# Performance work log

Measured on AMD Instinct MI355X. Metric: run time of the kernel, lower is better.

## Reference

```python
import jax, jax.numpy as jnp
import numpy as np
import math

B, D, S, C, H = 8192, 512, 5, 2048, 4

def setup_inputs() -> dict:
    key = jax.random.key(0)
    ks = jax.random.split(key, 8)
    return {
        "features": jax.random.normal(ks[0], (B, D), dtype=jnp.float32),
        "logits": jax.random.normal(ks[1], (S, B, C), dtype=jnp.float32),
        "scale_feats": jax.random.normal(ks[2], (S, B, D), dtype=jnp.float32),
        "Wq": jax.random.normal(ks[3], (D, D), dtype=jnp.float32) * 0.02,
        "bq": jnp.zeros((D,), jnp.float32),
        "Wk": jax.random.normal(ks[4], (D, D), dtype=jnp.float32) * 0.02,
        "bk": jnp.zeros((D,), jnp.float32),
        "Wv": jax.random.normal(ks[5], (D, D), dtype=jnp.float32) * 0.02,
        "bv": jnp.zeros((D,), jnp.float32),
        "scale_emb": jax.random.normal(ks[6], (S, D), dtype=jnp.float32) * 0.02,
        "temperature": jnp.float32(0.07),
        "attn_w": jnp.ones((3,), jnp.float32) / 3.0,
    }

def reference(features, logits, scale_feats, Wq, bq, Wk, bk, Wv, bv, scale_emb, temperature, attn_w):
    b, d = features.shape
    s = scale_feats.shape[0]
    hd = d // H
    t = jnp.abs(temperature)

    # ---- multihead attention over scales (V is computed in torch but unused) ----
    Q = (features @ Wq + bq).reshape(b, H, hd)                      # [B,H,hd]
    sf_emb = scale_feats + scale_emb[:, None, :]                    # [S,B,D]
    K = (sf_emb @ Wk + bk).reshape(s, b, H, hd)                     # [S,B,H,hd]
    scores = jnp.einsum('bhd,sbhd->bhs', Q, K) / jnp.float32(math.sqrt(hd))
    attn_mha = jax.nn.softmax(scores / t, axis=-1).mean(axis=1)     # [B,S]

    # ---- geometric (angular) attention ----
    fn = features / jnp.linalg.norm(features, axis=-1, keepdims=True).clip(1e-12)
    sfn = scale_feats / jnp.linalg.norm(scale_feats, axis=-1, keepdims=True).clip(1e-12)
    cos_sim = jnp.einsum('bd,sbd->bs', fn, sfn)                     # [B,S]
    angles = jnp.arccos(jnp.clip(cos_sim, -1.0 + 1e-7, 1.0 - 1e-7))
    attn_geo = jax.nn.softmax(jnp.exp(-angles / t), axis=-1)        # [B,S]

    # ---- Cayley-Menger volume-proxy attention ----
    # simplex points: [features, scale_feat, cos(a)*f + sin(a)*s for a in {pi/4, pi/2, 3pi/4}]
    c = jnp.float32(math.sqrt(0.5))
    cf = jnp.array([1.0, 0.0, c, 0.0, -c], jnp.float32)             # coeffs on features
    cs = jnp.array([0.0, 1.0, c, 1.0, c], jnp.float32)              # coeffs on scale_feat
    simplex = (cf[None, :, None, None] * features[None, None] +
               cs[None, :, None, None] * scale_feats[:, None])      # [S,5,B,D]
    norms = jnp.sum(simplex * simplex, axis=-1)                     # [S,5,B]
    gram = jnp.einsum('spbd,sqbd->spqb', simplex, simplex)          # [S,5,5,B]
    distsq = norms[:, :, None] + norms[:, None, :] - 2.0 * gram     # [S,5,5,B]
    volumes = distsq.mean(axis=(1, 2)).T                            # [B,S]
    attn_cay = jax.nn.softmax(volumes / t, axis=-1)

    # ---- fuse attention types ----
    w = jax.nn.softmax(attn_w, axis=0)
    combined = w[0] * attn_mha + w[1] * attn_geo + w[2] * attn_cay  # [B,S]
    combined = combined / combined.sum(axis=-1, keepdims=True)

    combined_logits = jnp.einsum('bs,sbc->bc', combined, logits)    # [B,C]
    return (combined_logits, combined)
```

## Files before the change

### kernel.cpp

```cpp
#include <hip/hip_runtime.h>
#include <math.h>

#define B_N 8192
#define D_N 512
#define S_N 5
#define C_N 2048
#define H_N 4

typedef __attribute__((ext_vector_type(8))) short bf16x8;
typedef __attribute__((ext_vector_type(4))) float floatx4;

__device__ __forceinline__ float bf2f(short u) {
  union { unsigned int i; float f; } c;
  c.i = ((unsigned int)(unsigned short)u) << 16;
  return c.f;
}
__device__ __forceinline__ short f2bf(float f) {
  union { float f; unsigned int i; } c; c.f = f;
  unsigned int x = c.i;
  x += 0x7fffu + ((x >> 16) & 1u);
  return (short)(x >> 16);
}

__global__ __launch_bounds__(256) void k_cvt_f(const float* __restrict__ f,
                                               short* __restrict__ fbf, int n8) {
  int i = blockIdx.x * 256 + threadIdx.x;
  if (i >= n8) return;
  const floatx4* p = (const floatx4*)(f + (size_t)i * 8);
  floatx4 a = p[0], b = p[1];
  bf16x8 o;
  o[0] = f2bf(a[0]); o[1] = f2bf(a[1]); o[2] = f2bf(a[2]); o[3] = f2bf(a[3]);
  o[4] = f2bf(b[0]); o[5] = f2bf(b[1]); o[6] = f2bf(b[2]); o[7] = f2bf(b[3]);
  *(bf16x8*)(fbf + (size_t)i * 8) = o;
}

__global__ __launch_bounds__(256) void k_cvt_w(const float* __restrict__ Wq,
                                               const float* __restrict__ Wk,
                                               short* __restrict__ WqT,
                                               short* __restrict__ Wkb) {
  int o = blockIdx.x * 256 + threadIdx.x;
  if (blockIdx.x < 1024) {
    int n = o >> 9, k = o & 511;
    WqT[(size_t)n * 512 + k] = f2bf(Wq[(size_t)k * 512 + n]);
  } else {
    int o2 = o - 262144;
    Wkb[o2] = f2bf(Wk[o2]);
  }
}

__device__ __forceinline__ void gll(const short* g, short* l) {
  __builtin_amdgcn_global_load_lds(
      (const __attribute__((address_space(1))) unsigned int*)(g),
      (__attribute__((address_space(3))) unsigned int*)(l), 16, 0, 0);
}

__global__ __launch_bounds__(256) void k_gemm(
    const short* __restrict__ A, int lda,
    const short* __restrict__ BT, int ldb,
    short* __restrict__ O, int ldo,
    const float* __restrict__ bias, int K, int z_koff, int z_coff) {
  __shared__ __align__(16) short As[2][4096];
  __shared__ __align__(16) short Bs[2][4096];

  const int tid = threadIdx.x;
  const int lane = tid & 63;
  const int wid = tid >> 6;
  const int wr = wid >> 1, wc = wid & 1;
  const int row0 = blockIdx.y * 128;
  const int col0 = blockIdx.x * 128;
  const int z = blockIdx.z;
  const int koff = z * z_koff;
  const int ocoff = z * z_coff;

  const int r1 = tid >> 2, hk = tid & 3;
  const short* Ag1 = A + (size_t)(row0 + r1) * lda + koff + hk * 8;
  const short* Ag2 = A + (size_t)(row0 + 64 + r1) * lda + koff + hk * 8;
  const short* Bg1 = BT + (size_t)(col0 + r1) * ldb + koff + hk * 8;
  const short* Bg2 = BT + (size_t)(col0 + 64 + r1) * ldb + koff + hk * 8;

  floatx4 acc[4][4];
  const floatx4 zero = {0.0f, 0.0f, 0.0f, 0.0f};
#pragma unroll
  for (int m = 0; m < 4; ++m)
#pragma unroll
    for (int n = 0; n < 4; ++n) acc[m][n] = zero;

  const int NT = K >> 5;
  int cur = 0;

  auto stage = [&](int q, int kb) {
    gll(Ag1 + kb, &As[q][tid * 8]);
    gll(Ag2 + kb, &As[q][tid * 8 + 2048]);
    gll(Bg1 + kb, &Bs[q][tid * 8]);
    gll(Bg2 + kb, &Bs[q][tid * 8 + 2048]);
  };

  stage(0, 0);
  __syncthreads();

  for (int t = 0; t < NT; ++t) {
    if (t + 1 < NT) stage(cur ^ 1, (t + 1) * 32);
    bf16x8 af[4], bfr[4];
#pragma unroll
    for (int m = 0; m < 4; ++m)
      af[m] = *(const bf16x8*)&As[cur][(wr * 64 + m * 16 + (lane & 15)) * 32 + (lane >> 4) * 8];
#pragma unroll
    for (int n = 0; n < 4; ++n)
      bfr[n] = *(const bf16x8*)&Bs[cur][(wc * 64 + n * 16 + (lane & 15)) * 32 + (lane >> 4) * 8];
#pragma unroll
    for (int m = 0; m < 4; ++m)
#pragma unroll
      for (int n = 0; n < 4; ++n)
        acc[m][n] = __builtin_amdgcn_mfma_f32_16x16x32_bf16(af[m], bfr[n], acc[m][n], 0, 0, 0);
    __syncthreads();
    cur ^= 1;
  }

#pragma unroll
  for (int m = 0; m < 4; ++m) {
    int rowb = row0 + wr * 64 + m * 16 + (lane >> 4) * 4;
#pragma unroll
    for (int n = 0; n < 4; ++n) {
      int lcol = col0 + wc * 64 + n * 16 + (lane & 15);
      float bv = bias ? bias[lcol] : 0.0f;
      int ocol = ocoff + lcol;
#pragma unroll
      for (int j = 0; j < 4; ++j) {
        O[(size_t)(rowb + j) * ldo + ocol] = f2bf(acc[m][n][j] + bv);
      }
    }
  }
}

__global__ __launch_bounds__(256) void k_stats(
    const float* __restrict__ f, const float* __restrict__ sf,
    const float* __restrict__ emb, const short* __restrict__ Qbf,
    const short* __restrict__ Rbf, const float* __restrict__ bk,
    const float* __restrict__ temp, const float* __restrict__ attn_w,
    float* __restrict__ comb_out) {
  const int lane = threadIdx.x & 63;
  const int wid = threadIdx.x >> 6;
  const int b = blockIdx.x * 4 + wid;
  const int a0 = lane * 8;

  const floatx4* fp = (const floatx4*)(f + (size_t)b * D_N + a0);
  floatx4 fA = fp[0], fB = fp[1];
  float fv[8];
#pragma unroll
  for (int j = 0; j < 4; ++j) { fv[j] = fA[j]; fv[4 + j] = fB[j]; }
  float ffp = 0;
#pragma unroll
  for (int j = 0; j < 8; ++j) ffp += fv[j] * fv[j];

  bf16x8 qv = *(const bf16x8*)(Qbf + (size_t)b * D_N + a0);
  float qbkp = 0;
#pragma unroll
  for (int j = 0; j < 8; ++j) qbkp += bf2f(qv[j]) * bk[a0 + j];

  float rf[H_N][8];
#pragma unroll
  for (int h = 0; h < H_N; ++h) {
    bf16x8 rv = *(const bf16x8*)(Rbf + (size_t)b * 2048 + h * 512 + a0);
#pragma unroll
    for (int j = 0; j < 8; ++j) rf[h][j] = bf2f(rv[j]);
  }

  const int myh = lane >> 4;
  float fs_[S_N], ss_[S_N], sc_[S_N][H_N];

#pragma unroll
  for (int s = 0; s < S_N; ++s) {
    const floatx4* sp = (const floatx4*)(sf + ((size_t)s * B_N + b) * D_N + a0);
    floatx4 sA = sp[0], sB = sp[1];
    const floatx4* ep = (const floatx4*)(emb + (size_t)s * D_N + a0);
    floatx4 eA = ep[0], eB = ep[1];
    float sv[8], se[8];
#pragma unroll
    for (int j = 0; j < 4; ++j) {
      sv[j] = sA[j]; sv[4 + j] = sB[j];
      se[j] = sA[j] + eA[j]; se[4 + j] = sB[j] + eB[j];
    }
    float fsp = 0, ssp = 0;
    float scp[H_N];
#pragma unroll
    for (int h = 0; h < H_N; ++h) scp[h] = (myh == h) ? qbkp : 0.0f;
#pragma unroll
    for (int j = 0; j < 8; ++j) {
      fsp += fv[j] * sv[j];
      ssp += sv[j] * sv[j];
#pragma unroll
      for (int h = 0; h < H_N; ++h) scp[h] += se[j] * rf[h][j];
    }
#pragma unroll
    for (int o = 1; o < 64; o <<= 1) {
      fsp += __shfl_xor(fsp, o, 64);
      ssp += __shfl_xor(ssp, o, 64);
#pragma unroll
      for (int h = 0; h < H_N; ++h) scp[h] += __shfl_xor(scp[h], o, 64);
    }
    fs_[s] = fsp; ss_[s] = ssp;
#pragma unroll
    for (int h = 0; h < H_N; ++h) sc_[s][h] = scp[h];
  }
  float ffv = ffp;
#pragma unroll
  for (int o = 1; o < 64; o <<= 1) ffv += __shfl_xor(ffv, o, 64);

  const float t = fabsf(temp[0]);

  float amha[S_N] = {0, 0, 0, 0, 0};
  const float inv_mha = 1.0f / (sqrtf(128.0f) * t);
#pragma unroll
  for (int h = 0; h < H_N; ++h) {
    float lg[S_N];
#pragma unroll
    for (int s = 0; s < S_N; ++s) lg[s] = sc_[s][h] * inv_mha;
    float mx = lg[0];
#pragma unroll
    for (int s = 1; s < S_N; ++s) mx = fmaxf(mx, lg[s]);
    float e[S_N], sum = 0;
#pragma unroll
    for (int s = 0; s < S_N; ++s) { e[s] = __expf(lg[s] - mx); sum += e[s]; }
    float isum = 0.25f / sum;
#pragma unroll
    for (int s = 0; s < S_N; ++s) amha[s] += e[s] * isum;
  }

  float ageo[S_N];
  {
    const float nf = fmaxf(sqrtf(ffv), 1e-12f);
    float g[S_N];
#pragma unroll
    for (int s = 0; s < S_N; ++s) {
      float ns = fmaxf(sqrtf(ss_[s]), 1e-12f);
      float cs0 = fs_[s] / (nf * ns);
      cs0 = fminf(fmaxf(cs0, -1.0f + 1e-7f), 1.0f - 1e-7f);
      g[s] = __expf(-acosf(cs0) / t);
    }
    float mx = g[0];
#pragma unroll
    for (int s = 1; s < S_N; ++s) mx = fmaxf(mx, g[s]);
    float sum = 0;
#pragma unroll
    for (int s = 0; s < S_N; ++s) { ageo[s] = __expf(g[s] - mx); sum += ageo[s]; }
#pragma unroll
    for (int s = 0; s < S_N; ++s) ageo[s] /= sum;
  }

  float acay[S_N];
  {
    const float SQ2 = 1.41421356237309515f;
    const float Aff = 0.72f;
    const float Ass = 0.72f - 0.32f * SQ2;
    const float Afs = -(8.0f + 4.0f * SQ2) / 25.0f;
    float lg[S_N];
#pragma unroll
    for (int s = 0; s < S_N; ++s)
      lg[s] = (Aff * ffv + Ass * ss_[s] + Afs * fs_[s]) / t;
    float mx = lg[0];
#pragma unroll
    for (int s = 1; s < S_N; ++s) mx = fmaxf(mx, lg[s]);
    float sum = 0;
#pragma unroll
    for (int s = 0; s < S_N; ++s) { acay[s] = __expf(lg[s] - mx); sum += acay[s]; }
#pragma unroll
    for (int s = 0; s < S_N; ++s) acay[s] /= sum;
  }

  float w0 = attn_w[0], w1 = attn_w[1], w2 = attn_w[2];
  float wm = fmaxf(w0, fmaxf(w1, w2));
  float e0 = __expf(w0 - wm), e1 = __expf(w1 - wm), e2 = __expf(w2 - wm);
  float wsum = e0 + e1 + e2;
  w0 = e0 / wsum; w1 = e1 / wsum; w2 = e2 / wsum;

  float cb[S_N], csum = 0;
#pragma unroll
  for (int s = 0; s < S_N; ++s) {
    cb[s] = w0 * amha[s] + w1 * ageo[s] + w2 * acay[s];
    csum += cb[s];
  }
  float ic = 1.0f / csum;
  if (lane == 0) {
#pragma unroll
    for (int s = 0; s < S_N; ++s) comb_out[(size_t)b * S_N + s] = cb[s] * ic;
  }
}

__global__ __launch_bounds__(256) void k_mix(const float* __restrict__ logits,
                                             const float* __restrict__ comb,
                                             float* __restrict__ out) {
  const int b = blockIdx.x;
  const int c0 = threadIdx.x * 8;
  float cs[S_N];
#pragma unroll
  for (int s = 0; s < S_N; ++s) cs[s] = comb[(size_t)b * S_N + s];
  floatx4 accA = {0, 0, 0, 0}, accB = {0, 0, 0, 0};
#pragma unroll
  for (int s = 0; s < S_N; ++s) {
    const float* lp = logits + ((size_t)s * B_N + b) * C_N + c0;
    floatx4 lA = *(const floatx4*)lp;
    floatx4 lB = *(const floatx4*)(lp + 4);
    accA += lA * cs[s];
    accB += lB * cs[s];
  }
  float* op = out + (size_t)b * C_N + c0;
  *(floatx4*)op = accA;
  *(floatx4*)(op + 4) = accB;
}

extern "C" void kernel_launch(void* const* d_in, const int* in_sizes, int n_in,
                              void* d_out, int out_size, void* d_ws, size_t ws_size,
                              hipStream_t stream) {
  const float* features = (const float*)d_in[0];
  const float* logits   = (const float*)d_in[1];
  const float* sf       = (const float*)d_in[2];
  const float* Wq       = (const float*)d_in[3];
  const float* bq       = (const float*)d_in[4];
  const float* Wk       = (const float*)d_in[5];
  const float* bk       = (const float*)d_in[6];
  const float* emb      = (const float*)d_in[9];
  const float* temp     = (const float*)d_in[10];
  const float* attn_w   = (const float*)d_in[11];

  float* out  = (float*)d_out;
  float* comb = out + (size_t)B_N * C_N;

  char* w = (char*)d_ws;
  short* fbf = (short*)(w);
  short* Qbf = (short*)(w + 8388608);
  short* Rbf = (short*)(w + 16777216);
  short* WqT = (short*)(w + 50331648);
  short* Wkb = (short*)(w + 50855936);

  k_cvt_f<<<dim3(2048), dim3(256), 0, stream>>>(features, fbf, 524288);
  k_cvt_w<<<dim3(2048), dim3(256), 0, stream>>>(Wq, Wk, WqT, Wkb);
  k_gemm<<<dim3(4, 64, 1), dim3(256), 0, stream>>>(fbf, 512, WqT, 512, Qbf, 512,
                                                   bq, 512, 0, 0);
  k_gemm<<<dim3(4, 64, 4), dim3(256), 0, stream>>>(Qbf, 512, Wkb, 512, Rbf, 2048,
                                                   (const float*)nullptr, 128, 128, 512);
  k_stats<<<dim3(2048), dim3(256), 0, stream>>>(features, sf, emb, Qbf, Rbf, bk,
                                                temp, attn_w, comb);
  k_mix<<<dim3(8192), dim3(256), 0, stream>>>(logits, comb, out);
}
```

Before: 158.4 us.

## Fuse feature conversion, both GEMMs and stats into one per-row-block kernel

Replaces the feature conversion, the Q GEMM, the Q·Wk^T GEMM and the stats kernel with a single kernel. Each block handles 32 rows, keeps the bf16 features and Q in swizzled LDS, and computes per-head K·Q scores on the fly against bf16 scale-feature tiles. This removes the global round-trips of fbf, Qbf and the large Rbf intermediate plus several launches. The cost is only 256 blocks with heavy LDS use and weight fragments read straight from global/L2 without LDS staging, so occupancy and GEMM efficiency may drop.

Measured after the change: 157.2 us. No clear change (-0.8%).

```diff
diff --git a/kernel.cpp b/kernel.cpp
--- a/kernel.cpp
+++ b/kernel.cpp
@@ -6,6 +6,7 @@
 #define S_N 5
 #define C_N 2048
 #define H_N 4
+#define RB 32
 
 typedef __attribute__((ext_vector_type(8))) short bf16x8;
 typedef __attribute__((ext_vector_type(4))) float floatx4;
@@ -21,23 +22,17 @@
   x += 0x7fffu + ((x >> 16) & 1u);
   return (short)(x >> 16);
 }
-
-__global__ __launch_bounds__(256) void k_cvt_f(const float* __restrict__ f,
-                                               short* __restrict__ fbf, int n8) {
-  int i = blockIdx.x * 256 + threadIdx.x;
-  if (i >= n8) return;
-  const floatx4* p = (const floatx4*)(f + (size_t)i * 8);
-  floatx4 a = p[0], b = p[1];
-  bf16x8 o;
-  o[0] = f2bf(a[0]); o[1] = f2bf(a[1]); o[2] = f2bf(a[2]); o[3] = f2bf(a[3]);
-  o[4] = f2bf(b[0]); o[5] = f2bf(b[1]); o[6] = f2bf(b[2]); o[7] = f2bf(b[3]);
-  *(bf16x8*)(fbf + (size_t)i * 8) = o;
-}
-
-__global__ __launch_bounds__(256) void k_cvt_w(const float* __restrict__ Wq,
-                                               const float* __restrict__ Wk,
-                                               short* __restrict__ WqT,
-                                               short* __restrict__ Wkb) {
+__device__ __forceinline__ unsigned long long pack4(float a, float b, float c, float d) {
+  return (unsigned long long)(unsigned short)f2bf(a)
+       | ((unsigned long long)(unsigned short)f2bf(b) << 16)
+       | ((unsigned long long)(unsigned short)f2bf(c) << 32)
+       | ((unsigned long long)(unsigned short)f2bf(d) << 48);
+}
+
+__global__ __launch_bounds__(256) void k_prep(const float* __restrict__ Wq,
+                                              const float* __restrict__ Wk,
+                                              short* __restrict__ WqT,
+                                              short* __restrict__ Wkb) {
   int o = blockIdx.x * 256 + threadIdx.x;
   if (blockIdx.x < 1024) {
     int n = o >> 9, k = o & 511;
@@ -48,241 +43,318 @@
   }
 }
 
-__device__ __forceinline__ void gll(const short* g, short* l) {
-  __builtin_amdgcn_global_load_lds(
-      (const __attribute__((address_space(1))) unsigned int*)(g),
-      (__attribute__((address_space(3))) unsigned int*)(l), 16, 0, 0);
-}
-
-__global__ __launch_bounds__(256) void k_gemm(
-    const short* __restrict__ A, int lda,
-    const short* __restrict__ BT, int ldb,
-    short* __restrict__ O, int ldo,
-    const float* __restrict__ bias, int K, int z_koff, int z_coff) {
-  __shared__ __align__(16) short As[2][4096];
-  __shared__ __align__(16) short Bs[2][4096];
+__global__ __launch_bounds__(256, 2) void k_mega(
+    const float* __restrict__ f, const float* __restrict__ sf,
+    const float* __restrict__ emb, const short* __restrict__ WqT,
+    const short* __restrict__ Wkb, const float* __restrict__ bq,
+    const float* __restrict__ bk, const float* __restrict__ temp,
+    const float* __restrict__ attn_w, float* __restrict__ comb_out) {
+  __shared__ __align__(16) short uni[21120];
+  __shared__ __align__(16) short Qbf[16384];
+  __shared__ float ffLds[RB];
+  __shared__ float qtLds[RB][H_N];
+  __shared__ float scLds[RB][H_N][S_N];
+  __shared__ float fsLds[S_N][RB];
+  __shared__ float ssLds[S_N][RB];
 
   const int tid = threadIdx.x;
   const int lane = tid & 63;
   const int wid = tid >> 6;
-  const int wr = wid >> 1, wc = wid & 1;
-  const int row0 = blockIdx.y * 128;
-  const int col0 = blockIdx.x * 128;
-  const int z = blockIdx.z;
-  const int koff = z * z_koff;
-  const int ocoff = z * z_coff;
-
-  const int r1 = tid >> 2, hk = tid & 3;
-  const short* Ag1 = A + (size_t)(row0 + r1) * lda + koff + hk * 8;
-  const short* Ag2 = A + (size_t)(row0 + 64 + r1) * lda + koff + hk * 8;
-  const short* Bg1 = BT + (size_t)(col0 + r1) * ldb + koff + hk * 8;
-  const short* Bg2 = BT + (size_t)(col0 + 64 + r1) * ldb + koff + hk * 8;
-
-  floatx4 acc[4][4];
-  const floatx4 zero = {0.0f, 0.0f, 0.0f, 0.0f};
-#pragma unroll
-  for (int m = 0; m < 4; ++m)
-#pragma unroll
-    for (int n = 0; n < 4; ++n) acc[m][n] = zero;
-
-  const int NT = K >> 5;
-  int cur = 0;
-
-  auto stage = [&](int q, int kb) {
-    gll(Ag1 + kb, &As[q][tid * 8]);
-    gll(Ag2 + kb, &As[q][tid * 8 + 2048]);
-    gll(Bg1 + kb, &Bs[q][tid * 8]);
-    gll(Bg2 + kb, &Bs[q][tid * 8 + 2048]);
-  };
-
-  stage(0, 0);
+  const int b0 = blockIdx.x * RB;
+
+  {
+    const int r0 = tid >> 3;
+    const int c0 = (tid & 7) * 64;
+    const float* fp = f + (size_t)(b0 + r0) * D_N + c0;
+    float ffp = 0.0f;
+#pragma unroll
+    for (int i = 0; i < 8; ++i) {
+      floatx4 a = *(const floatx4*)(fp + i * 8);
+      floatx4 b = *(const floatx4*)(fp + i * 8 + 4);
+      ffp += a[0]*a[0] + a[1]*a[1] + a[2]*a[2] + a[3]*a[3];
+      ffp += b[0]*b[0] + b[1]*b[1] + b[2]*b[2] + b[3]*b[3];
+      bf16x8 o;
+      o[0]=f2bf(a[0]); o[1]=f2bf(a[1]); o[2]=f2bf(a[2]); o[3]=f2bf(a[3]);
+      o[4]=f2bf(b[0]); o[5]=f2bf(b[1]); o[6]=f2bf(b[2]); o[7]=f2bf(b[3]);
+      int byteoff = (r0 * 1024 + (c0 + i * 8) * 2) ^ ((r0 & 7) << 4);
+      *(bf16x8*)((char*)uni + byteoff) = o;
+    }
+    ffp += __shfl_xor(ffp, 1, 64);
+    ffp += __shfl_xor(ffp, 2, 64);
+    ffp += __shfl_xor(ffp, 4, 64);
+    if ((tid & 7) == 0) ffLds[r0] = ffp;
+  }
   __syncthreads();
 
-  for (int t = 0; t < NT; ++t) {
-    if (t + 1 < NT) stage(cur ^ 1, (t + 1) * 32);
-    bf16x8 af[4], bfr[4];
-#pragma unroll
-    for (int m = 0; m < 4; ++m)
-      af[m] = *(const bf16x8*)&As[cur][(wr * 64 + m * 16 + (lane & 15)) * 32 + (lane >> 4) * 8];
-#pragma unroll
-    for (int n = 0; n < 4; ++n)
-      bfr[n] = *(const bf16x8*)&Bs[cur][(wc * 64 + n * 16 + (lane & 15)) * 32 + (lane >> 4) * 8];
-#pragma unroll
-    for (int m = 0; m < 4; ++m)
-#pragma unroll
-      for (int n = 0; n < 4; ++n)
-        acc[m][n] = __builtin_amdgcn_mfma_f32_16x16x32_bf16(af[m], bfr[n], acc[m][n], 0, 0, 0);
+  {
+    const int wcol0 = wid * 128;
+    floatx4 acc[2][8];
+    const floatx4 zero = {0.f, 0.f, 0.f, 0.f};
+#pragma unroll
+    for (int m = 0; m < 2; ++m)
+#pragma unroll
+      for (int n = 0; n < 8; ++n) acc[m][n] = zero;
+
+    for (int ks = 0; ks < 16; ++ks) {
+      bf16x8 bfr[8];
+#pragma unroll
+      for (int n = 0; n < 8; ++n) {
+        int col = wcol0 + n * 16 + (lane & 15);
+        bfr[n] = *(const bf16x8*)(WqT + (size_t)col * 512 + ks * 32 + (lane >> 4) * 8);
+      }
+      bf16x8 afr[2];
+#pragma unroll
+      for (int m = 0; m < 2; ++m) {
+        int row = m * 16 + (lane & 15);
+        int byteoff = (row * 1024 + (ks * 32 + (lane >> 4) * 8) * 2) ^ ((row & 7) << 4);
+        afr[m] = *(const bf16x8*)((const char*)uni + byteoff);
+      }
+#pragma unroll
+      for (int m = 0; m < 2; ++m)
+#pragma unroll
+        for (int n = 0; n < 8; ++n)
+          acc[m][n] = __builtin_amdgcn_mfma_f32_16x16x32_bf16(afr[m], bfr[n], acc[m][n], 0, 0, 0);
+    }
+
+    float bqv[8], bkv[8];
+#pragma unroll
+    for (int n = 0; n < 8; ++n) {
+      int col = wcol0 + n * 16 + (lane & 15);
+      bqv[n] = bq[col];
+      bkv[n] = bk[col];
+    }
+#pragma unroll
+    for (int m = 0; m < 2; ++m) {
+#pragma unroll
+      for (int j = 0; j < 4; ++j) {
+        int row = m * 16 + (lane >> 4) * 4 + j;
+        float qp = 0.0f;
+#pragma unroll
+        for (int n = 0; n < 8; ++n) {
+          float qv = acc[m][n][j] + bqv[n];
+          int col = wcol0 + n * 16 + (lane & 15);
+          int byteoff = (row * 1024 + col * 2) ^ ((row & 7) << 4);
+          *(short*)((char*)Qbf + byteoff) = f2bf(qv);
+          qp += qv * bkv[n];
+        }
+        qp += __shfl_xor(qp, 1, 64);
+        qp += __shfl_xor(qp, 2, 64);
+        qp += __shfl_xor(qp, 4, 64);
+        qp += __shfl_xor(qp, 8, 64);
+        if ((lane & 15) == 0) qtLds[row][wid] = qp;
+      }
+    }
+  }
+  __syncthreads();
+
+  float scp[S_N][2][4];
+#pragma unroll
+  for (int s = 0; s < S_N; ++s)
+#pragma unroll
+    for (int m = 0; m < 2; ++m)
+#pragma unroll
+      for (int j = 0; j < 4; ++j) scp[s][m][j] = 0.0f;
+  float ssp[S_N] = {0, 0, 0, 0, 0}, fsp[S_N] = {0, 0, 0, 0, 0};
+
+  const int h = wid;
+  for (int cc = 0; cc < 4; ++cc) {
+    {
+      const int r1 = tid >> 3;
+      const int cs0 = (tid & 7) * 16;
+      const int ac0 = cc * 128 + cs0;
+      const float* fpp = f + (size_t)(b0 + r1) * D_N + ac0;
+      float fsl[16];
+#pragma unroll
+      for (int i = 0; i < 4; ++i) {
+        floatx4 v = *(const floatx4*)(fpp + i * 4);
+        fsl[i * 4 + 0] = v[0]; fsl[i * 4 + 1] = v[1];
+        fsl[i * 4 + 2] = v[2]; fsl[i * 4 + 3] = v[3];
+      }
+#pragma unroll
+      for (int s = 0; s < S_N; ++s) {
+        const float* sp = sf + ((size_t)s * B_N + b0 + r1) * D_N + ac0;
+        const float* ep = emb + s * D_N + ac0;
+        float sv[16], se[16];
+#pragma unroll
+        for (int i = 0; i < 4; ++i) {
+          floatx4 a = *(const floatx4*)(sp + i * 4);
+          floatx4 e = *(const floatx4*)(ep + i * 4);
+#pragma unroll
+          for (int q = 0; q < 4; ++q) {
+            sv[i * 4 + q] = a[q];
+            se[i * 4 + q] = a[q] + e[q];
+          }
+        }
+        float ssl = 0.0f, fsll = 0.0f;
+#pragma unroll
+        for (int q = 0; q < 16; ++q) { ssl += sv[q] * sv[q]; fsll += fsl[q] * sv[q]; }
+        ssp[s] += ssl; fsp[s] += fsll;
+        int rowbase = (s * RB + r1) * 264 + cs0 * 2;
+#pragma unroll
+        for (int q = 0; q < 4; ++q) {
+          unsigned long long pk = pack4(se[q*4], se[q*4+1], se[q*4+2], se[q*4+3]);
+          *(unsigned long long*)((char*)uni + rowbase + q * 8) = pk;
+        }
+      }
+    }
     __syncthreads();
-    cur ^= 1;
-  }
-
-#pragma unroll
-  for (int m = 0; m < 4; ++m) {
-    int rowb = row0 + wr * 64 + m * 16 + (lane >> 4) * 4;
-#pragma unroll
-    for (int n = 0; n < 4; ++n) {
-      int lcol = col0 + wc * 64 + n * 16 + (lane & 15);
-      float bv = bias ? bias[lcol] : 0.0f;
-      int ocol = ocoff + lcol;
+
+    {
+      floatx4 acc2[2][8];
+      const floatx4 zero = {0.f, 0.f, 0.f, 0.f};
+#pragma unroll
+      for (int m = 0; m < 2; ++m)
+#pragma unroll
+        for (int n = 0; n < 8; ++n) acc2[m][n] = zero;
+
+#pragma unroll
+      for (int ks = 0; ks < 4; ++ks) {
+        bf16x8 bfr[8];
+#pragma unroll
+        for (int n = 0; n < 8; ++n) {
+          int a = cc * 128 + n * 16 + (lane & 15);
+          bfr[n] = *(const bf16x8*)(Wkb + (size_t)a * 512 + h * 128 + ks * 32 + (lane >> 4) * 8);
+        }
+        bf16x8 afr[2];
+#pragma unroll
+        for (int m = 0; m < 2; ++m) {
+          int row = m * 16 + (lane & 15);
+          int byteoff = (row * 1024 + (h * 128 + ks * 32 + (lane >> 4) * 8) * 2) ^ ((row & 7) << 4);
+          afr[m] = *(const bf16x8*)((const char*)Qbf + byteoff);
+        }
+#pragma unroll
+        for (int m = 0; m < 2; ++m)
+#pragma unroll
+          for (int n = 0; n < 8; ++n)
+            acc2[m][n] = __builtin_amdgcn_mfma_f32_16x16x32_bf16(afr[m], bfr[n], acc2[m][n], 0, 0, 0);
+      }
+#pragma unroll
+      for (int s = 0; s < S_N; ++s) {
+#pragma unroll
+        for (int m = 0; m < 2; ++m) {
+#pragma unroll
+          for (int j = 0; j < 4; ++j) {
+            int row = m * 16 + (lane >> 4) * 4 + j;
+            int base = (s * RB + row) * 264 + (lane & 15) * 2;
+            float p = 0.0f;
+#pragma unroll
+            for (int n = 0; n < 8; ++n) {
+              short sv = *(const short*)((const char*)uni + base + n * 32);
+              p += acc2[m][n][j] * bf2f(sv);
+            }
+            scp[s][m][j] += p;
+          }
+        }
+      }
+    }
+    __syncthreads();
+  }
+
+#pragma unroll
+  for (int s = 0; s < S_N; ++s)
+#pragma unroll
+    for (int m = 0; m < 2; ++m)
 #pragma unroll
       for (int j = 0; j < 4; ++j) {
-        O[(size_t)(rowb + j) * ldo + ocol] = f2bf(acc[m][n][j] + bv);
-      }
-    }
-  }
-}
-
-__global__ __launch_bounds__(256) void k_stats(
-    const float* __restrict__ f, const float* __restrict__ sf,
-    const float* __restrict__ emb, const short* __restrict__ Qbf,
-    const short* __restrict__ Rbf, const float* __restrict__ bk,
-    const float* __restrict__ temp, const float* __restrict__ attn_w,
-    float* __restrict__ comb_out) {
-  const int lane = threadIdx.x & 63;
-  const int wid = threadIdx.x >> 6;
-  const int b = blockIdx.x * 4 + wid;
-  const int a0 = lane * 8;
-
-  const floatx4* fp = (const floatx4*)(f + (size_t)b * D_N + a0);
-  floatx4 fA = fp[0], fB = fp[1];
-  float fv[8];
-#pragma unroll
-  for (int j = 0; j < 4; ++j) { fv[j] = fA[j]; fv[4 + j] = fB[j]; }
-  float ffp = 0;
-#pragma unroll
-  for (int j = 0; j < 8; ++j) ffp += fv[j] * fv[j];
-
-  bf16x8 qv = *(const bf16x8*)(Qbf + (size_t)b * D_N + a0);
-  float qbkp = 0;
-#pragma unroll
-  for (int j = 0; j < 8; ++j) qbkp += bf2f(qv[j]) * bk[a0 + j];
-
-  float rf[H_N][8];
-#pragma unroll
-  for (int h = 0; h < H_N; ++h) {
-    bf16x8 rv = *(const bf16x8*)(Rbf + (size_t)b * 2048 + h * 512 + a0);
-#pragma unroll
-    for (int j = 0; j < 8; ++j) rf[h][j] = bf2f(rv[j]);
-  }
-
-  const int myh = lane >> 4;
-  float fs_[S_N], ss_[S_N], sc_[S_N][H_N];
-
-#pragma unroll
-  for (int s = 0; s < S_N; ++s) {
-    const floatx4* sp = (const floatx4*)(sf + ((size_t)s * B_N + b) * D_N + a0);
-    floatx4 sA = sp[0], sB = sp[1];
-    const floatx4* ep = (const floatx4*)(emb + (size_t)s * D_N + a0);
-    floatx4 eA = ep[0], eB = ep[1];
-    float sv[8], se[8];
-#pragma unroll
-    for (int j = 0; j < 4; ++j) {
-      sv[j] = sA[j]; sv[4 + j] = sB[j];
-      se[j] = sA[j] + eA[j]; se[4 + j] = sB[j] + eB[j];
-    }
-    float fsp = 0, ssp = 0;
-    float scp[H_N];
-#pragma unroll
-    for (int h = 0; h < H_N; ++h) scp[h] = (myh == h) ? qbkp : 0.0f;
-#pragma unroll
-    for (int j = 0; j < 8; ++j) {
-      fsp += fv[j] * sv[j];
-      ssp += sv[j] * sv[j];
-#pragma unroll
-      for (int h = 0; h < H_N; ++h) scp[h] += se[j] * rf[h][j];
-    }
-#pragma unroll
-    for (int o = 1; o < 64; o <<= 1) {
-      fsp += __shfl_xor(fsp, o, 64);
-      ssp += __shfl_xor(ssp, o, 64);
-#pragma unroll
-      for (int h = 0; h < H_N; ++h) scp[h] += __shfl_xor(scp[h], o, 64);
-    }
-    fs_[s] = fsp; ss_[s] = ssp;
-#pragma unroll
-    for (int h = 0; h < H_N; ++h) sc_[s][h] = scp[h];
-  }
-  float ffv = ffp;
-#pragma unroll
-  for (int o = 1; o < 64; o <<= 1) ffv += __shfl_xor(ffv, o, 64);
-
-  const float t = fabsf(temp[0]);
-
-  float amha[S_N] = {0, 0, 0, 0, 0};
-  const float inv_mha = 1.0f / (sqrtf(128.0f) * t);
-#pragma unroll
-  for (int h = 0; h < H_N; ++h) {
-    float lg[S_N];
-#pragma unroll
-    for (int s = 0; s < S_N; ++s) lg[s] = sc_[s][h] * inv_mha;
-    float mx = lg[0];
-#pragma unroll
-    for (int s = 1; s < S_N; ++s) mx = fmaxf(mx, lg[s]);
-    float e[S_N], sum = 0;
-#pragma unroll
-    for (int s = 0; s < S_N; ++s) { e[s] = __expf(lg[s] - mx); sum += e[s]; }
-    float isum = 0.25f / sum;
-#pragma unroll
-    for (int s = 0; s < S_N; ++s) amha[s] += e[s] * isum;
-  }
-
-  float ageo[S_N];
+        float v = scp[s][m][j];
+        v += __shfl_xor(v, 1, 64);
+        v += __shfl_xor(v, 2, 64);
+        v += __shfl_xor(v, 4, 64);
+        v += __shfl_xor(v, 8, 64);
+        if ((lane & 15) == 0) scLds[m * 16 + (lane >> 4) * 4 + j][wid][s] = v;
+      }
   {
-    const float nf = fmaxf(sqrtf(ffv), 1e-12f);
-    float g[S_N];
+    const int r1 = tid >> 3;
 #pragma unroll
     for (int s = 0; s < S_N; ++s) {
-      float ns = fmaxf(sqrtf(ss_[s]), 1e-12f);
-      float cs0 = fs_[s] / (nf * ns);
-      cs0 = fminf(fmaxf(cs0, -1.0f + 1e-7f), 1.0f - 1e-7f);
-      g[s] = __expf(-acosf(cs0) / t);
-    }
-    float mx = g[0];
-#pragma unroll
-    for (int s = 1; s < S_N; ++s) mx = fmaxf(mx, g[s]);
-    float sum = 0;
-#pragma unroll
-    for (int s = 0; s < S_N; ++s) { ageo[s] = __expf(g[s] - mx); sum += ageo[s]; }
-#pragma unroll
-    for (int s = 0; s < S_N; ++s) ageo[s] /= sum;
-  }
-
-  float acay[S_N];
-  {
-    const float SQ2 = 1.41421356237309515f;
-    const float Aff = 0.72f;
-    const float Ass = 0.72f - 0.32f * SQ2;
-    const float Afs = -(8.0f + 4.0f * SQ2) / 25.0f;
-    float lg[S_N];
-#pragma unroll
-    for (int s = 0; s < S_N; ++s)
-      lg[s] = (Aff * ffv + Ass * ss_[s] + Afs * fs_[s]) / t;
-    float mx = lg[0];
-#pragma unroll
-    for (int s = 1; s < S_N; ++s) mx = fmaxf(mx, lg[s]);
-    float sum = 0;
-#pragma unroll
-    for (int s = 0; s < S_N; ++s) { acay[s] = __expf(lg[s] - mx); sum += acay[s]; }
-#pragma unroll
-    for (int s = 0; s < S_N; ++s) acay[s] /= sum;
-  }
-
-  float w0 = attn_w[0], w1 = attn_w[1], w2 = attn_w[2];
-  float wm = fmaxf(w0, fmaxf(w1, w2));
-  float e0 = __expf(w0 - wm), e1 = __expf(w1 - wm), e2 = __expf(w2 - wm);
-  float wsum = e0 + e1 + e2;
-  w0 = e0 / wsum; w1 = e1 / wsum; w2 = e2 / wsum;
-
-  float cb[S_N], csum = 0;
-#pragma unroll
-  for (int s = 0; s < S_N; ++s) {
-    cb[s] = w0 * amha[s] + w1 * ageo[s] + w2 * acay[s];
-    csum += cb[s];
-  }
-  float ic = 1.0f / csum;
-  if (lane == 0) {
-#pragma unroll
-    for (int s = 0; s < S_N; ++s) comb_out[(size_t)b * S_N + s] = cb[s] * ic;
+      float u = ssp[s], v = fsp[s];
+      u += __shfl_xor(u, 1, 64); v += __shfl_xor(v, 1, 64);
+      u += __shfl_xor(u, 2, 64); v += __shfl_xor(v, 2, 64);
+      u += __shfl_xor(u, 4, 64); v += __shfl_xor(v, 4, 64);
+      if ((tid & 7) == 0) { ssLds[s][r1] = u; fsLds[s][r1] = v; }
+    }
+  }
+  __syncthreads();
+
+  if (tid < RB) {
+    const int r = tid;
+    const float ffv = ffLds[r];
+    const float t = fabsf(temp[0]);
+
+    float amha[S_N] = {0, 0, 0, 0, 0};
+    const float inv_mha = 1.0f / (sqrtf(128.0f) * t);
+#pragma unroll
+    for (int hh = 0; hh < H_N; ++hh) {
+      float lg[S_N];
+#pragma unroll
+      for (int s = 0; s < S_N; ++s) lg[s] = (scLds[r][hh][s] + qtLds[r][hh]) * inv_mha;
+      float mx = lg[0];
+#pragma unroll
+      for (int s = 1; s < S_N; ++s) mx = fmaxf(mx, lg[s]);
+      float e[S_N], sum = 0;
+#pragma unroll
+      for (int s = 0; s < S_N; ++s) { e[s] = __expf(lg[s] - mx); sum += e[s]; }
+      float isum = 0.25f / sum;
+#pragma unroll
+      for (int s = 0; s < S_N; ++s) amha[s] += e[s] * isum;
+    }
+
+    float ageo[S_N];
+    {
+      const float nf = fmaxf(sqrtf(ffv), 1e-12f);
+      float g[S_N];
+#pragma unroll
+      for (int s = 0; s < S_N; ++s) {
+        float ns = fmaxf(sqrtf(ssLds[s][r]), 1e-12f);
+        float cs0 = fsLds[s][r] / (nf * ns);
+        cs0 = fminf(fmaxf(cs0, -1.0f + 1e-7f), 1.0f - 1e-7f);
+        g[s] = __expf(-acosf(cs0) / t);
+      }
+      float mx = g[0];
+#pragma unroll
+      for (int s = 1; s < S_N; ++s) mx = fmaxf(mx, g[s]);
+      float sum = 0;
+#pragma unroll
+      for (int s = 0; s < S_N; ++s) { ageo[s] = __expf(g[s] - mx); sum += ageo[s]; }
+#pragma unroll
+      for (int s = 0; s < S_N; ++s) ageo[s] /= sum;
+    }
+
+    float acay[S_N];
+    {
+      const float SQ2 = 1.41421356237309515f;
+      const float Aff = 0.72f;
+      const float Ass = 0.72f - 0.32f * SQ2;
+      const float Afs = -(8.0f + 4.0f * SQ2) / 25.0f;
+      float lg[S_N];
+#pragma unroll
+      for (int s = 0; s < S_N; ++s)
+        lg[s] = (Aff * ffv + Ass * ssLds[s][r] + Afs * fsLds[s][r]) / t;
+      float mx = lg[0];
+#pragma unroll
+      for (int s = 1; s < S_N; ++s) mx = fmaxf(mx, lg[s]);
+      float sum = 0;
+#pragma unroll
+      for (int s = 0; s < S_N; ++s) { acay[s] = __expf(lg[s] - mx); sum += acay[s]; }
+#pragma unroll
+      for (int s = 0; s < S_N; ++s) acay[s] /= sum;
+    }
+
+    float w0 = attn_w[0], w1 = attn_w[1], w2 = attn_w[2];
+    float wm = fmaxf(w0, fmaxf(w1, w2));
+    float e0 = __expf(w0 - wm), e1 = __expf(w1 - wm), e2 = __expf(w2 - wm);
+    float wsum = e0 + e1 + e2;
+    w0 = e0 / wsum; w1 = e1 / wsum; w2 = e2 / wsum;
+
+    float cb[S_N], csum = 0;
+#pragma unroll
+    for (int s = 0; s < S_N; ++s) {
+      cb[s] = w0 * amha[s] + w1 * ageo[s] + w2 * acay[s];
+      csum += cb[s];
+    }
+    float ic = 1.0f / csum;
+#pragma unroll
+    for (int s = 0; s < S_N; ++s) comb_out[(size_t)(b0 + r) * S_N + s] = cb[s] * ic;
   }
 }
 
@@ -316,7 +388,7 @@
   const float* sf       = (const float*)d_in[2];
   const float* Wq       = (const float*)d_in[3];
   const float* bq       = (const float*)d_in[4];
-  const float* Wk       = (const float*)d_in[5];
+  const float* Wk       = (const float*)d_in[6 - 1];
   const float* bk       = (const float*)d_in[6];
   const float* emb      = (const float*)d_in[9];
   const float* temp     = (const float*)d_in[10];
@@ -326,19 +398,11 @@
   float* comb = out + (size_t)B_N * C_N;
 
   char* w = (char*)d_ws;
-  short* fbf = (short*)(w);
-  short* Qbf = (short*)(w + 8388608);
-  short* Rbf = (short*)(w + 16777216);
-  short* WqT = (short*)(w + 50331648);
-  short* Wkb = (short*)(w + 50855936);
-
-  k_cvt_f<<<dim3(2048), dim3(256), 0, stream>>>(features, fbf, 524288);
-  k_cvt_w<<<dim3(2048), dim3(256), 0, stream>>>(Wq, Wk, WqT, Wkb);
-  k_gemm<<<dim3(4, 64, 1), dim3(256), 0, stream>>>(fbf, 512, WqT, 512, Qbf, 512,
-                                                   bq, 512, 0, 0);
-  k_gemm<<<dim3(4, 64, 4), dim3(256), 0, stream>>>(Qbf, 512, Wkb, 512, Rbf, 2048,
-                                                   (const float*)nullptr, 128, 128, 512);
-  k_stats<<<dim3(2048), dim3(256), 0, stream>>>(features, sf, emb, Qbf, Rbf, bk,
-                                                temp, attn_w, comb);
+  short* WqT = (short*)(w);
+  short* Wkb = (short*)(w + 524288);
+
+  k_prep<<<dim3(2048), dim3(256), 0, stream>>>(Wq, Wk, WqT, Wkb);
+  k_mega<<<dim3(256), dim3(256), 0, stream>>>(features, sf, emb, WqT, Wkb, bq, bk,
+                                              temp, attn_w, comb);
   k_mix<<<dim3(8192), dim3(256), 0, stream>>>(logits, comb, out);
 }
```

## Fuse logit mixing into stats kernel and tile the weight transpose through LDS

Applied to the files above, without the earlier changes.

The separate mixing kernel is folded into the per-row stats kernel, so each wave blends the five logit rows right after computing its combined weights, skipping one launch and the round trip through the comb buffer. The weight-prep kernel now transposes Wq through a padded LDS tile for coalesced accesses and converts Wk with vectorized loads and packed bf16 stores. The fused kernel carries more work and register pressure per wave, so launch_bounds asks for 4 blocks per SM. The logit stream (about 335 MB read plus 67 MB written) is memory-bound either way.

Result: no change. 159.0 us (+0.4%).

```diff
diff --git a/kernel.cpp b/kernel.cpp
--- a/kernel.cpp
+++ b/kernel.cpp
@@ -20,6 +20,12 @@
   unsigned int x = c.i;
   x += 0x7fffu + ((x >> 16) & 1u);
   return (short)(x >> 16);
+}
+__device__ __forceinline__ unsigned long long pack4(float a, float b, float c, float d) {
+  return (unsigned long long)(unsigned short)f2bf(a)
+       | ((unsigned long long)(unsigned short)f2bf(b) << 16)
+       | ((unsigned long long)(unsigned short)f2bf(c) << 32)
+       | ((unsigned long long)(unsigned short)f2bf(d) << 48);
 }
 
 __global__ __launch_bounds__(256) void k_cvt_f(const float* __restrict__ f,
@@ -34,17 +40,33 @@
   *(bf16x8*)(fbf + (size_t)i * 8) = o;
 }
 
-__global__ __launch_bounds__(256) void k_cvt_w(const float* __restrict__ Wq,
-                                               const float* __restrict__ Wk,
-                                               short* __restrict__ WqT,
-                                               short* __restrict__ Wkb) {
-  int o = blockIdx.x * 256 + threadIdx.x;
-  if (blockIdx.x < 1024) {
-    int n = o >> 9, k = o & 511;
-    WqT[(size_t)n * 512 + k] = f2bf(Wq[(size_t)k * 512 + n]);
+__global__ __launch_bounds__(256) void k_prep(const float* __restrict__ Wq,
+                                              const float* __restrict__ Wk,
+                                              short* __restrict__ WqT,
+                                              short* __restrict__ Wkb) {
+  __shared__ float lds[64][65];
+  const int bx = blockIdx.x, t = threadIdx.x;
+  if (bx < 64) {
+    const int r0 = (bx >> 3) * 64, c0 = (bx & 7) * 64;
+#pragma unroll
+    for (int i = 0; i < 16; ++i) {
+      int r = i * 4 + (t >> 6), c = t & 63;
+      lds[r][c] = Wq[(size_t)(r0 + r) * 512 + c0 + c];
+    }
+    __syncthreads();
+#pragma unroll
+    for (int i = 0; i < 16; ++i) {
+      int cL = i * 4 + (t >> 6), rL = t & 63;
+      WqT[(size_t)(c0 + cL) * 512 + r0 + rL] = f2bf(lds[rL][cL]);
+    }
   } else {
-    int o2 = o - 262144;
-    Wkb[o2] = f2bf(Wk[o2]);
+    const int base = (bx - 64) * 8192 + t * 4;
+#pragma unroll
+    for (int i = 0; i < 8; ++i) {
+      int idx = base + i * 1024;
+      floatx4 v = *(const floatx4*)(Wk + idx);
+      *(unsigned long long*)(Wkb + idx) = pack4(v[0], v[1], v[2], v[3]);
+    }
   }
 }
 
@@ -132,11 +154,12 @@
   }
 }
 
-__global__ __launch_bounds__(256) void k_stats(
+__global__ __launch_bounds__(256, 4) void k_fused(
     const float* __restrict__ f, const float* __restrict__ sf,
     const float* __restrict__ emb, const short* __restrict__ Qbf,
     const short* __restrict__ Rbf, const float* __restrict__ bk,
     const float* __restrict__ temp, const float* __restrict__ attn_w,
+    const float* __restrict__ logits, float* __restrict__ out,
     float* __restrict__ comb_out) {
   const int lane = threadIdx.x & 63;
   const int wid = threadIdx.x >> 6;
@@ -280,32 +303,31 @@
     csum += cb[s];
   }
   float ic = 1.0f / csum;
+  float cbn[S_N];
+#pragma unroll
+  for (int s = 0; s < S_N; ++s) cbn[s] = cb[s] * ic;
   if (lane == 0) {
 #pragma unroll
-    for (int s = 0; s < S_N; ++s) comb_out[(size_t)b * S_N + s] = cb[s] * ic;
-  }
-}
-
-__global__ __launch_bounds__(256) void k_mix(const float* __restrict__ logits,
-                                             const float* __restrict__ comb,
-                                             float* __restrict__ out) {
-  const int b = blockIdx.x;
-  const int c0 = threadIdx.x * 8;
-  float cs[S_N];
-#pragma unroll
-  for (int s = 0; s < S_N; ++s) cs[s] = comb[(size_t)b * S_N + s];
-  floatx4 accA = {0, 0, 0, 0}, accB = {0, 0, 0, 0};
-#pragma unroll
-  for (int s = 0; s < S_N; ++s) {
-    const float* lp = logits + ((size_t)s * B_N + b) * C_N + c0;
-    floatx4 lA = *(const floatx4*)lp;
-    floatx4 lB = *(const floatx4*)(lp + 4);
-    accA += lA * cs[s];
-    accB += lB * cs[s];
-  }
-  float* op = out + (size_t)b * C_N + c0;
-  *(floatx4*)op = accA;
-  *(floatx4*)(op + 4) = accB;
+    for (int s = 0; s < S_N; ++s) comb_out[(size_t)b * S_N + s] = cbn[s];
+  }
+
+  const floatx4 fz = {0.f, 0.f, 0.f, 0.f};
+#pragma unroll
+  for (int cj = 0; cj < 4; ++cj) {
+    const int c0 = cj * 512 + lane * 8;
+    floatx4 accA = fz, accB = fz;
+#pragma unroll
+    for (int s = 0; s < S_N; ++s) {
+      const float* lp = logits + ((size_t)s * B_N + b) * C_N + c0;
+      floatx4 lA = *(const floatx4*)lp;
+      floatx4 lB = *(const floatx4*)(lp + 4);
+      accA += lA * cbn[s];
+      accB += lB * cbn[s];
+    }
+    float* op = out + (size_t)b * C_N + c0;
+    *(floatx4*)op = accA;
+    *(floatx4*)(op + 4) = accB;
+  }
 }
 
 extern "C" void kernel_launch(void* const* d_in, const int* in_sizes, int n_in,
@@ -333,12 +355,11 @@
   short* Wkb = (short*)(w + 50855936);
 
   k_cvt_f<<<dim3(2048), dim3(256), 0, stream>>>(features, fbf, 524288);
-  k_cvt_w<<<dim3(2048), dim3(256), 0, stream>>>(Wq, Wk, WqT, Wkb);
+  k_prep<<<dim3(96), dim3(256), 0, stream>>>(Wq, Wk, WqT, Wkb);
   k_gemm<<<dim3(4, 64, 1), dim3(256), 0, stream>>>(fbf, 512, WqT, 512, Qbf, 512,
                                                    bq, 512, 0, 0);
   k_gemm<<<dim3(4, 64, 4), dim3(256), 0, stream>>>(Qbf, 512, Wkb, 512, Rbf, 2048,
                                                    (const float*)nullptr, 128, 128, 512);
-  k_stats<<<dim3(2048), dim3(256), 0, stream>>>(features, sf, emb, Qbf, Rbf, bk,
-                                                temp, attn_w, comb);
-  k_mix<<<dim3(8192), dim3(256), 0, stream>>>(logits, comb, out);
-}
+  k_fused<<<dim3(2048), dim3(256), 0, stream>>>(features, sf, emb, Qbf, Rbf, bk,
+                                                temp, attn_w, logits, out, comb);
+}
```
